# Optimization experiments

Hardware: AMD Instinct MI355X
Metric: run time of the kernel (lower is better)

Reference implementation:

```python
import jax, jax.numpy as jnp
import numpy as np

GW_EPS = 0.05
GW_SIGMA = 1.0
GW_OUTER_ITERS = 5
GW_SINK_ITERS = 20
N_HEADS = 8
EPS = 1e-8


def normalize_affinity(P):
    # symmetrize, scale to [0,1]
    P = 0.5 * (P + jnp.swapaxes(P, -1, -2))
    mx = jnp.max(P, axis=(-2, -1), keepdims=True)
    return P / jnp.maximum(mx, EPS)


def entropic_gw(C1, C2, a, b, eps, outer_iters, sink_iters):
    # C1: [B,H,S,S] node-space cost, C2: [B,H,K,K] slot-space cost
    # a: [B,H,S], b: [B,H,K] marginals. Square-loss entropic GW (Peyre et al.)
    T = a[..., :, None] * b[..., None, :]                      # [B,H,S,K]
    cC1 = jnp.einsum('bhij,bhj->bhi', C1 * C1, a)              # [B,H,S]
    cC2 = jnp.einsum('bhk,bhkl->bhl', b, C2 * C2)              # [B,H,K]
    const = cC1[..., :, None] + cC2[..., None, :]              # [B,H,S,K]
    tens = const
    for _ in range(outer_iters):
        tens = const - 2.0 * jnp.einsum('bhis,bhsk,bhlk->bhil', C1, T, C2)
        Kmat = jnp.exp(-tens / eps)
        u = jnp.ones_like(a)
        v = jnp.ones_like(b)
        def sink_step(carry, _):
            u, v = carry
            u = a / jnp.maximum(jnp.einsum('bhik,bhk->bhi', Kmat, v), 1e-30)
            v = b / jnp.maximum(jnp.einsum('bhik,bhi->bhk', Kmat, u), 1e-30)
            return (u, v), None
        (u, v), _ = jax.lax.scan(sink_step, (u, v), None, length=sink_iters)
        T = u[..., :, None] * Kmat * v[..., None, :]
    gw_val = jnp.sum(tens * T, axis=(-2, -1))                  # [B,H]
    return T, gw_val


def _forward(desc_embeddings, name_value_embeddings, shared_attn, prior_Q, DG, b, v_w, v_b):
    B, new_seq, D = name_value_embeddings.shape
    S = new_seq - 1
    H = N_HEADS
    hd = D // H

    # structural adjacency: CLS->Var on, Var->CLS off, Var-Var without self-loop
    var_adj = 1.0 - jnp.eye(S, dtype=name_value_embeddings.dtype)
    adj = jnp.zeros((new_seq, new_seq), dtype=name_value_embeddings.dtype)
    adj = adj.at[1:, 1:].set(var_adj)
    adj = adj.at[0, 1:].set(1.0)

    # Var-Var affinity from shared attention (detached in original)
    P_var = jax.lax.stop_gradient(shared_attn[:, :, 1:, 1:])   # [B,H,S,S]
    P_norm = normalize_affinity(P_var)
    DP = 1.0 - P_norm                                          # affinity -> distance

    deg_P = 0.5 * (P_norm.sum(-1) + P_norm.sum(-2))            # [B,H,S]
    a = deg_P / jnp.maximum(deg_P.sum(-1, keepdims=True), EPS)

    _, gw_val = entropic_gw(DP, DG, a, b, GW_EPS, GW_OUTER_ITERS, GW_SINK_ITERS)
    alpha = jnp.exp(-gw_val / GW_SIGMA)                        # [B,H] in (0,1]

    # sharpen prior Q by alpha (power sharpening + row renorm)
    Q_hat = jnp.power(jnp.maximum(prior_Q, EPS), 1.0 + alpha[..., None, None])
    Q_hat = Q_hat / jnp.maximum(Q_hat.sum(-1, keepdims=True), EPS)

    # embed Q_hat into CLS-augmented attention, mask, row-normalize
    slot = jnp.zeros((B, H, new_seq, new_seq), dtype=Q_hat.dtype)
    slot = slot.at[:, :, 1:, 1:].set(Q_hat)
    slot = slot.at[:, :, 0, 1:].set(1.0)
    slot = slot * adj[None, None]
    attn = slot / jnp.maximum(slot.sum(-1, keepdims=True), EPS)  # [B,H,S1,S1]

    v = name_value_embeddings @ v_w.T + v_b                    # [B,S1,D]
    v = v.reshape(B, new_seq, H, hd).transpose(0, 2, 1, 3)     # [B,H,S1,hd]
    context = jnp.einsum('bhij,bhjd->bhid', attn, v)
    basis_outputs = context.transpose(0, 2, 1, 3)              # [B,S1,H,hd]
    return basis_outputs, attn


def setup_inputs() -> dict:
    key = jax.random.key(0)
    ks = jax.random.split(key, 8)
    B, S1, D, H, K = 32, 385, 256, 8, 16
    S = S1 - 1
    desc = jax.random.normal(ks[0], (B, S, D), jnp.float32)
    nv = jax.random.normal(ks[1], (B, S1, D), jnp.float32)
    shared_attn = jax.nn.softmax(jax.random.normal(ks[2], (B, H, S1, S1), jnp.float32), axis=-1)
    prior_Q = jax.nn.softmax(jax.random.normal(ks[3], (B, H, S, S), jnp.float32), axis=-1)
    DG = jax.random.uniform(ks[4], (B, H, K, K), jnp.float32)
    DG = 0.5 * (DG + jnp.swapaxes(DG, -1, -2))
    b = jax.random.uniform(ks[5], (B, H, K), jnp.float32) + 0.1
    b = b / b.sum(-1, keepdims=True)
    v_w = jax.random.normal(ks[6], (D, D), jnp.float32) * (1.0 / np.sqrt(D))
    v_b = jnp.zeros((D,), jnp.float32)
    return {"desc_embeddings": desc, "name_value_embeddings": nv, "shared_attn": shared_attn,
            "prior_Q": prior_Q, "DG": DG, "b": b, "v_w": v_w, "v_b": v_b}


def reference(desc_embeddings, name_value_embeddings, shared_attn, prior_Q, DG, b, v_w, v_b):
    return _forward(desc_embeddings, name_value_embeddings, shared_attn, prior_Q, DG, b, v_w, v_b)
```

## Files before the change

kernel.cpp:

```cpp
#include <hip/hip_runtime.h>
#include <math.h>

constexpr int kS  = 384;
constexpr int kS1 = 385;
constexpr int kH  = 8;
constexpr int kB  = 32;
constexpr int kD  = 256;
constexpr float kEPS = 1e-8f;
constexpr float kNEG_INV_EPS_LOG2E = 28.853900817779268f;

__device__ __forceinline__ float waveReduceSum(float v) {
    #pragma unroll
    for (int m = 1; m < 64; m <<= 1) v += __shfl_xor(v, m);
    return v;
}
__device__ __forceinline__ float waveReduceMax(float v) {
    #pragma unroll
    for (int m = 1; m < 64; m <<= 1) v = fmaxf(v, __shfl_xor(v, m));
    return v;
}

__global__ __launch_bounds__(384) void k1_gw(
    const float* __restrict__ shared_attn,
    const float* __restrict__ DG,
    const float* __restrict__ bmarg,
    float* __restrict__ sym_ws,
    float* __restrict__ alpha_out)
{
    const int head = blockIdx.x;
    const int tid  = threadIdx.x;
    const int lane = tid & 63, wid = tid >> 6;

    __shared__ __align__(16) float uni[8320];
    __shared__ float Ks[kS * 17];
    __shared__ float ravu[kS];
    __shared__ float part[16 * 24];
    __shared__ float C2l[256];
    __shared__ float bl16[16], cb16[16], cC216[16], vls[16];
    __shared__ float wred[6];

    float* tA = uni;
    float* tB = uni + 4160;
    float* Ms = uni;

    const float* P = shared_attn + (size_t)head * (kS1 * kS1);
    float* SYM = sym_ws + (size_t)head * (kS1 * kS1);

    ravu[tid] = 0.f;
    if (tid < 256) C2l[tid] = DG[head * 256 + tid];
    if (tid >= 256 && tid < 272) bl16[tid - 256] = bmarg[head * 16 + (tid - 256)];
    __syncthreads();

    float mymax = -1e30f;
    for (int ti = 0; ti < 6; ++ti)
    for (int tj = ti; tj < 6; ++tj) {
        for (int e = tid; e < 4096; e += 384) {
            int r = e >> 6, c = e & 63;
            tA[r * 65 + c] = P[(ti * 64 + r + 1) * kS1 + (tj * 64 + c + 1)];
            tB[r * 65 + c] = P[(tj * 64 + r + 1) * kS1 + (ti * 64 + c + 1)];
        }
        __syncthreads();
        for (int e = tid; e < 4096; e += 384) {
            int r = e >> 6, c = e & 63;
            float v = 0.5f * (tA[r * 65 + c] + tB[c * 65 + r]);
            tA[r * 65 + c] = v;
            mymax = fmaxf(mymax, v);
        }
        __syncthreads();
        for (int e = tid; e < 4096; e += 384) {
            int r = e >> 6, c = e & 63;
            SYM[(ti * 64 + r) * kS + tj * 64 + c] = tA[r * 65 + c];
        }
        if (ti != tj) {
            for (int e = tid; e < 4096; e += 384) {
                int r = e >> 6, c = e & 63;
                SYM[(tj * 64 + r) * kS + ti * 64 + c] = tA[c * 65 + r];
            }
        }
        if (tid < 64) {
            int r = tid; float s = 0.f;
            #pragma unroll 8
            for (int c = 0; c < 64; ++c) s += tA[r * 65 + c];
            ravu[ti * 64 + r] += s;
        } else if (tid < 128 && ti != tj) {
            int c = tid - 64; float s = 0.f;
            #pragma unroll 8
            for (int r = 0; r < 64; ++r) s += tA[r * 65 + c];
            ravu[tj * 64 + c] += s;
        }
        __syncthreads();
    }

    float wm = waveReduceMax(mymax);
    if (lane == 0) wred[wid] = wm;
    __syncthreads();
    const float mx = fmaxf(fmaxf(fmaxf(wred[0], wred[1]), fmaxf(wred[2], wred[3])),
                           fmaxf(wred[4], wred[5]));
    float tloc = ravu[tid];
    float tw = waveReduceSum(tloc);
    __syncthreads();
    if (lane == 0) wred[wid] = tw;
    __syncthreads();
    const float total = wred[0] + wred[1] + wred[2] + wred[3] + wred[4] + wred[5];

    const float den_mx = fmaxf(mx, kEPS);
    const float inv_mx = 1.0f / den_mx;
    const float Sdeg   = total * inv_mx;
    const float den_a  = fmaxf(Sdeg, kEPS);
    const float a_reg  = (tloc * inv_mx) / den_a;
    __syncthreads();
    ravu[tid] = a_reg;

    if (tid < 16) {
        float cb = 0.f, cc2 = 0.f;
        #pragma unroll
        for (int k = 0; k < 16; ++k) {
            cb += bl16[k] * C2l[tid * 16 + k];
            float c2 = C2l[k * 16 + tid];
            cc2 = fmaf(bl16[k] * c2, c2, cc2);
        }
        cb16[tid] = cb; cC216[tid] = cc2;
    }
    __syncthreads();

    float t1 = 0.f, t2 = 0.f;
    {
        const float* symcol = SYM + tid;
        #pragma unroll 4
        for (int s = 0; s < kS; ++s) {
            float sym = symcol[s * kS];
            float dp  = fmaf(-inv_mx, sym, 1.0f);
            float as  = ravu[s];
            t1 = fmaf(dp, as, t1);
            t2 = fmaf(dp * dp, as, t2);
        }
    }
    const float cc1 = t2;
    #pragma unroll
    for (int l = 0; l < 16; ++l) {
        float tens = cc1 + cC216[l] - 2.0f * cb16[l] * t1;
        Ks[tid * 17 + l] = exp2f(tens * (-kNEG_INV_EPS_LOG2E));
    }

    float vreg[16];
    float u_i = 0.f;

    auto sinkhorn = [&]() {
        #pragma unroll
        for (int l = 0; l < 16; ++l) vreg[l] = 1.0f;
        for (int it = 0; it < 20; ++it) {
            float su = 0.f;
            #pragma unroll
            for (int l = 0; l < 16; ++l) su = fmaf(Ks[tid * 17 + l], vreg[l], su);
            u_i = a_reg / fmaxf(su, 1e-30f);
            ravu[tid] = u_i;
            __syncthreads();
            {
                int l = tid & 15, g = tid >> 4;
                float sv = 0.f;
                #pragma unroll
                for (int j = 0; j < 16; ++j)
                    sv = fmaf(Ks[(g * 16 + j) * 17 + l], ravu[g * 16 + j], sv);
                part[l * 24 + g] = sv;
            }
            __syncthreads();
            if (tid < 16) {
                float dn = 0.f;
                #pragma unroll
                for (int g = 0; g < 24; ++g) dn += part[tid * 24 + g];
                vls[tid] = bl16[tid] / fmaxf(dn, 1e-30f);
            }
            __syncthreads();
            #pragma unroll
            for (int l = 0; l < 16; ++l) vreg[l] = vls[l];
        }
    };

    __syncthreads();
    sinkhorn();

    float tens16[16];
    #pragma unroll
    for (int l = 0; l < 16; ++l) tens16[l] = 0.f;

    for (int outer = 1; outer < 5; ++outer) {
        {
            float wk[16];
            #pragma unroll
            for (int k = 0; k < 16; ++k) wk[k] = Ks[tid * 17 + k] * vreg[k];
            float m[16];
            #pragma unroll
            for (int l = 0; l < 16; ++l) {
                float acc = 0.f;
                #pragma unroll
                for (int k = 0; k < 16; ++k) acc = fmaf(wk[k], C2l[l * 16 + k], acc);
                m[l] = acc * u_i;
            }
            float4* Ms4 = (float4*)Ms;
            Ms4[tid * 4 + 0] = make_float4(m[0],  m[1],  m[2],  m[3]);
            Ms4[tid * 4 + 1] = make_float4(m[4],  m[5],  m[6],  m[7]);
            Ms4[tid * 4 + 2] = make_float4(m[8],  m[9],  m[10], m[11]);
            Ms4[tid * 4 + 3] = make_float4(m[12], m[13], m[14], m[15]);
        }
        __syncthreads();
        float rd[16];
        #pragma unroll
        for (int l = 0; l < 16; ++l) rd[l] = 0.f;
        {
            const float* symcol = SYM + tid;
            const float4* Ms4 = (const float4*)Ms;
            #pragma unroll 2
            for (int s = 0; s < kS; ++s) {
                float sym = symcol[s * kS];
                float dp  = fmaf(-inv_mx, sym, 1.0f);
                float4 m0 = Ms4[s * 4 + 0];
                float4 m1 = Ms4[s * 4 + 1];
                float4 m2 = Ms4[s * 4 + 2];
                float4 m3 = Ms4[s * 4 + 3];
                rd[0]  = fmaf(dp, m0.x, rd[0]);  rd[1]  = fmaf(dp, m0.y, rd[1]);
                rd[2]  = fmaf(dp, m0.z, rd[2]);  rd[3]  = fmaf(dp, m0.w, rd[3]);
                rd[4]  = fmaf(dp, m1.x, rd[4]);  rd[5]  = fmaf(dp, m1.y, rd[5]);
                rd[6]  = fmaf(dp, m1.z, rd[6]);  rd[7]  = fmaf(dp, m1.w, rd[7]);
                rd[8]  = fmaf(dp, m2.x, rd[8]);  rd[9]  = fmaf(dp, m2.y, rd[9]);
                rd[10] = fmaf(dp, m2.z, rd[10]); rd[11] = fmaf(dp, m2.w, rd[11]);
                rd[12] = fmaf(dp, m3.x, rd[12]); rd[13] = fmaf(dp, m3.y, rd[13]);
                rd[14] = fmaf(dp, m3.z, rd[14]); rd[15] = fmaf(dp, m3.w, rd[15]);
            }
        }
        #pragma unroll
        for (int l = 0; l < 16; ++l) {
            float tens = cc1 + cC216[l] - 2.0f * rd[l];
            if (outer == 4) tens16[l] = tens;
            Ks[tid * 17 + l] = exp2f(tens * (-kNEG_INV_EPS_LOG2E));
        }
        __syncthreads();
        sinkhorn();
    }

    float g = 0.f;
    #pragma unroll
    for (int l = 0; l < 16; ++l)
        g = fmaf(tens16[l] * Ks[tid * 17 + l], vreg[l], g);
    g *= u_i;
    float gww = waveReduceSum(g);
    __syncthreads();
    if (lane == 0) wred[wid] = gww;
    __syncthreads();
    if (tid == 0) {
        float gw = wred[0] + wred[1] + wred[2] + wred[3] + wred[4] + wred[5];
        alpha_out[head] = expf(-gw);
    }
}

__global__ __launch_bounds__(256) void k2_attn(
    const float* __restrict__ priorQ,
    const float* __restrict__ alpha_in,
    float* __restrict__ attn_out)
{
    const int tid  = threadIdx.x;
    const int lane = tid & 63, wid = tid >> 6;
    const int head = blockIdx.x / 97;
    const int i    = (blockIdx.x % 97) * 4 + wid;
    if (i >= kS1) return;
    float* row = attn_out + (size_t)head * (kS1 * kS1) + (size_t)i * kS1;
    if (i == 0) {
        const float val = 1.0f / 384.0f;
        for (int j = lane; j < kS1; j += 64) row[j] = (j == 0) ? 0.f : val;
        return;
    }
    const float e = 1.0f + alpha_in[head];
    const float* q = priorQ + (size_t)head * (kS * kS) + (size_t)(i - 1) * kS;
    float p[6];
    float loc = 0.f, locd = 0.f;
    #pragma unroll
    for (int k = 0; k < 6; ++k) {
        int j = lane + k * 64;
        float qv = fmaxf(q[j], kEPS);
        float pv = exp2f(e * log2f(qv));
        p[k] = pv;
        loc += pv;
        if (j == i - 1) locd = pv;
    }
    float sum = loc, pd = locd;
    #pragma unroll
    for (int m = 1; m < 64; m <<= 1) { sum += __shfl_xor(sum, m); pd += __shfl_xor(pd, m); }
    const float qsum  = fmaxf(sum, kEPS);
    const float srow  = (sum - pd) / qsum;
    const float scale = 1.0f / (qsum * fmaxf(srow, kEPS));
    if (lane == 0) row[0] = 0.f;
    #pragma unroll
    for (int k = 0; k < 6; ++k) {
        int j = lane + k * 64;
        row[1 + j] = (j == i - 1) ? 0.f : p[k] * scale;
    }
}

__global__ __launch_bounds__(256) void k3_vproj(
    const float* __restrict__ nv,
    const float* __restrict__ vw,
    const float* __restrict__ vb,
    float* __restrict__ vfull)
{
    __shared__ float At[64][17];
    __shared__ float Bt[256][17];
    const int tid = threadIdx.x;
    const int r0  = blockIdx.x * 64;
    const int tx  = tid & 31;
    const int ty  = tid >> 5;
    const int M   = kB * kS1;
    float acc[8][8];
    #pragma unroll
    for (int ri = 0; ri < 8; ++ri)
        #pragma unroll
        for (int ci = 0; ci < 8; ++ci) acc[ri][ci] = 0.f;

    for (int k0 = 0; k0 < 256; k0 += 16) {
        __syncthreads();
        for (int e = tid; e < 1024; e += 256) {
            int r = e >> 4, kk = e & 15;
            int rowi = r0 + r;
            At[r][kk] = (rowi < M) ? nv[rowi * 256 + k0 + kk] : 0.f;
        }
        for (int e = tid; e < 4096; e += 256) {
            int c = e >> 4, kk = e & 15;
            Bt[c][kk] = vw[c * 256 + k0 + kk];
        }
        __syncthreads();
        #pragma unroll
        for (int kk = 0; kk < 16; ++kk) {
            float av[8], bv[8];
            #pragma unroll
            for (int ri = 0; ri < 8; ++ri) av[ri] = At[ty * 8 + ri][kk];
            #pragma unroll
            for (int ci = 0; ci < 8; ++ci) bv[ci] = Bt[tx + 32 * ci][kk];
            #pragma unroll
            for (int ri = 0; ri < 8; ++ri)
                #pragma unroll
                for (int ci = 0; ci < 8; ++ci)
                    acc[ri][ci] = fmaf(av[ri], bv[ci], acc[ri][ci]);
        }
    }
    for (int ri = 0; ri < 8; ++ri) {
        int rowi = r0 + ty * 8 + ri;
        if (rowi < M) {
            #pragma unroll
            for (int ci = 0; ci < 8; ++ci) {
                int c = tx + 32 * ci;
                vfull[rowi * 256 + c] = acc[ri][ci] + vb[c];
            }
        }
    }
}

__global__ __launch_bounds__(256) void k4_ctx(
    const float* __restrict__ attn,
    const float* __restrict__ vfull,
    float* __restrict__ basis)
{
    __shared__ __align__(16) float at[8 * 32 * 28];
    __shared__ float vt[24 * 256];
    const int tid = threadIdx.x;
    const int bb  = blockIdx.y;
    const int i0  = blockIdx.x * 32;
    const int h   = tid >> 5;
    float acc[32];
    #pragma unroll
    for (int i = 0; i < 32; ++i) acc[i] = 0.f;
    const float* attnB = attn + (size_t)bb * kH * kS1 * kS1;
    const float* vB    = vfull + (size_t)bb * kS1 * 256;

    for (int j0 = 0; j0 < kS1; j0 += 24) {
        __syncthreads();
        for (int e = tid; e < 6144; e += 256) {
            int jj = e % 24, ii = (e / 24) & 31, hh = e / (24 * 32);
            int gi = i0 + ii, gj = j0 + jj;
            float v = (gi < kS1 && gj < kS1)
                      ? attnB[(size_t)hh * kS1 * kS1 + (size_t)gi * kS1 + gj] : 0.f;
            at[(hh * 32 + ii) * 28 + jj] = v;
        }
        for (int e = tid; e < 6144; e += 256) {
            int c = e & 255, jr = e >> 8;
            int gj = j0 + jr;
            vt[jr * 256 + c] = (gj < kS1) ? vB[gj * 256 + c] : 0.f;
        }
        __syncthreads();
        #pragma unroll
        for (int j4 = 0; j4 < 6; ++j4) {
            float v0 = vt[(j4 * 4 + 0) * 256 + tid];
            float v1 = vt[(j4 * 4 + 1) * 256 + tid];
            float v2 = vt[(j4 * 4 + 2) * 256 + tid];
            float v3 = vt[(j4 * 4 + 3) * 256 + tid];
            #pragma unroll
            for (int i = 0; i < 32; ++i) {
                float4 av = *(const float4*)&at[(h * 32 + i) * 28 + j4 * 4];
                acc[i] = fmaf(av.x, v0, fmaf(av.y, v1, fmaf(av.z, v2, fmaf(av.w, v3, acc[i]))));
            }
        }
    }
    for (int i = 0; i < 32; ++i) {
        int gi = i0 + i;
        if (gi < kS1) basis[((size_t)bb * kS1 + gi) * 256 + tid] = acc[i];
    }
}

extern "C" void kernel_launch(void* const* d_in, const int* in_sizes, int n_in,
                              void* d_out, int out_size, void* d_ws, size_t ws_size,
                              hipStream_t stream) {
    (void)in_sizes; (void)n_in; (void)out_size; (void)ws_size;
    const float* nv    = (const float*)d_in[1];
    const float* sattn = (const float*)d_in[2];
    const float* pq    = (const float*)d_in[3];
    const float* dg    = (const float*)d_in[4];
    const float* bm    = (const float*)d_in[5];
    const float* vw    = (const float*)d_in[6];
    const float* vb    = (const float*)d_in[7];

    float* out   = (float*)d_out;
    float* basis = out;
    float* attn  = out + (size_t)kB * kS1 * kD;
    float* alpha = (float*)d_ws;
    float* vfull = (float*)((char*)d_ws + 4096);

    k1_gw<<<256, 384, 0, stream>>>(sattn, dg, bm, attn, alpha);
    k2_attn<<<256 * 97, 256, 0, stream>>>(pq, alpha, attn);
    k3_vproj<<<193, 256, 0, stream>>>(nv, vw, vb, vfull);
    k4_ctx<<<dim3(13, 32), 256, 0, stream>>>(attn, vfull, basis);
}
```

Measured before the change: 1.336 ms.

## Split per-head GW solver into multi-block kernels and retile context matmul

The monolithic per-head GW kernel becomes several launches. Symmetrization runs over 21 tile pairs per head, with the max and row sums combined through atomics. The SYM-column reductions (t1/t2, and rd for each outer iteration) are split over 4 blocks per head with atomic accumulation, and a small per-head solve kernel runs Sinkhorn between them. The initial t1/cc1 are rewritten algebraically from raw sums of SYM and SYM². k4_ctx is also retiled per head with 4x4 register blocking. This spreads the memory-bound SYM streaming over far more blocks than 256, at the cost of more launches, memsets, atomics, and scratch stored in the output buffer before it is overwritten.

```diff
diff --git a/kernel.cpp b/kernel.cpp
--- a/kernel.cpp
+++ b/kernel.cpp
@@ -20,97 +20,137 @@
     return v;
 }
 
-__global__ __launch_bounds__(384) void k1_gw(
-    const float* __restrict__ shared_attn,
-    const float* __restrict__ DG,
-    const float* __restrict__ bmarg,
-    float* __restrict__ sym_ws,
-    float* __restrict__ alpha_out)
+__global__ __launch_bounds__(256) void kA_sym(
+    const float* __restrict__ P_, float* __restrict__ sym,
+    float* __restrict__ r_ws, unsigned int* __restrict__ mxbits)
+{
+    const int head = blockIdx.y;
+    int p = blockIdx.x, ti = 0;
+    while (p >= 6 - ti) { p -= 6 - ti; ++ti; }
+    const int tj = ti + p;
+    const int tid = threadIdx.x;
+    __shared__ float Bt[64 * 65];
+    __shared__ float St[64 * 65];
+    const float* P = P_ + (size_t)head * (kS1 * kS1);
+    float* SYM = sym + (size_t)head * (kS1 * kS1);
+
+    #pragma unroll
+    for (int e = tid; e < 4096; e += 256) {
+        int rr = e >> 6, cc = e & 63;
+        Bt[rr * 65 + cc] = P[(size_t)(tj * 64 + rr + 1) * kS1 + ti * 64 + cc + 1];
+    }
+    __syncthreads();
+    float mymax = 0.f;
+    #pragma unroll
+    for (int e = tid; e < 4096; e += 256) {
+        int rr = e >> 6, cc = e & 63;
+        float s = 0.5f * (P[(size_t)(ti * 64 + rr + 1) * kS1 + tj * 64 + cc + 1] + Bt[cc * 65 + rr]);
+        St[rr * 65 + cc] = s;
+        mymax = fmaxf(mymax, s);
+        SYM[(size_t)(ti * 64 + rr) * kS + tj * 64 + cc] = s;
+    }
+    __syncthreads();
+    if (ti != tj) {
+        #pragma unroll
+        for (int e = tid; e < 4096; e += 256) {
+            int rr = e >> 6, cc = e & 63;
+            SYM[(size_t)(tj * 64 + rr) * kS + ti * 64 + cc] = St[cc * 65 + rr];
+        }
+    }
+    float wm = waveReduceMax(mymax);
+    if ((tid & 63) == 0) atomicMax(mxbits + head, __float_as_uint(wm));
+    if (tid < 64) {
+        float s = 0.f;
+        #pragma unroll 8
+        for (int c = 0; c < 64; ++c) s += St[tid * 65 + c];
+        atomicAdd(r_ws + head * kS + ti * 64 + tid, s);
+    } else if (tid < 128 && ti != tj) {
+        int c = tid - 64; float s = 0.f;
+        #pragma unroll 8
+        for (int rr2 = 0; rr2 < 64; ++rr2) s += St[rr2 * 65 + c];
+        atomicAdd(r_ws + head * kS + tj * 64 + c, s);
+    }
+}
+
+__global__ __launch_bounds__(384) void kB_t(
+    const float* __restrict__ sym, const float* __restrict__ r_ws,
+    float* __restrict__ s1acc, float* __restrict__ s2acc)
+{
+    const int head = blockIdx.y;
+    const int s0 = blockIdx.x * 96;
+    const int tid = threadIdx.x;
+    __shared__ float rs[96];
+    if (tid < 96) rs[tid] = r_ws[head * kS + s0 + tid];
+    __syncthreads();
+    const float* SYM = sym + (size_t)head * (kS1 * kS1) + (size_t)s0 * kS + tid;
+    float s1 = 0.f, s2 = 0.f;
+    #pragma unroll 4
+    for (int k = 0; k < 96; ++k) {
+        float sy = SYM[(size_t)k * kS];
+        float rv = rs[k];
+        s1 = fmaf(sy, rv, s1);
+        s2 = fmaf(sy * sy, rv, s2);
+    }
+    atomicAdd(s1acc + head * kS + tid, s1);
+    atomicAdd(s2acc + head * kS + tid, s2);
+}
+
+__global__ __launch_bounds__(384) void kD_stream(
+    const float* __restrict__ sym, const float* __restrict__ Ms,
+    const unsigned int* __restrict__ mxbits, float* __restrict__ rd_acc)
+{
+    const int head = blockIdx.y;
+    const int s0 = blockIdx.x * 96;
+    const int tid = threadIdx.x;
+    __shared__ __align__(16) float MsS[96 * 16];
+    ((float4*)MsS)[tid] = ((const float4*)(Ms + (size_t)head * 6144 + s0 * 16))[tid];
+    __syncthreads();
+    const float inv_mx = 1.0f / fmaxf(__uint_as_float(mxbits[head]), kEPS);
+    const float* SYM = sym + (size_t)head * (kS1 * kS1) + (size_t)s0 * kS + tid;
+    float rd[16];
+    #pragma unroll
+    for (int l = 0; l < 16; ++l) rd[l] = 0.f;
+    const float4* Ms4 = (const float4*)MsS;
+    #pragma unroll 2
+    for (int k = 0; k < 96; ++k) {
+        float dp = fmaf(-inv_mx, SYM[(size_t)k * kS], 1.0f);
+        float4 m0 = Ms4[k * 4 + 0];
+        float4 m1 = Ms4[k * 4 + 1];
+        float4 m2 = Ms4[k * 4 + 2];
+        float4 m3 = Ms4[k * 4 + 3];
+        rd[0]  = fmaf(dp, m0.x, rd[0]);  rd[1]  = fmaf(dp, m0.y, rd[1]);
+        rd[2]  = fmaf(dp, m0.z, rd[2]);  rd[3]  = fmaf(dp, m0.w, rd[3]);
+        rd[4]  = fmaf(dp, m1.x, rd[4]);  rd[5]  = fmaf(dp, m1.y, rd[5]);
+        rd[6]  = fmaf(dp, m1.z, rd[6]);  rd[7]  = fmaf(dp, m1.w, rd[7]);
+        rd[8]  = fmaf(dp, m2.x, rd[8]);  rd[9]  = fmaf(dp, m2.y, rd[9]);
+        rd[10] = fmaf(dp, m2.z, rd[10]); rd[11] = fmaf(dp, m2.w, rd[11]);
+        rd[12] = fmaf(dp, m3.x, rd[12]); rd[13] = fmaf(dp, m3.y, rd[13]);
+        rd[14] = fmaf(dp, m3.z, rd[14]); rd[15] = fmaf(dp, m3.w, rd[15]);
+    }
+    float* dst = rd_acc + (size_t)head * 6144 + tid * 16;
+    #pragma unroll
+    for (int l = 0; l < 16; ++l) atomicAdd(dst + l, rd[l]);
+}
+
+__global__ __launch_bounds__(384) void kSolve(
+    const float* __restrict__ DG, const float* __restrict__ bmarg,
+    float* __restrict__ a_ws, const unsigned int* __restrict__ mxbits,
+    float* __restrict__ cc1_ws, const float* __restrict__ s2acc,
+    float* __restrict__ rd_acc, float* __restrict__ Ms,
+    float* __restrict__ alpha_out, int mode)
 {
     const int head = blockIdx.x;
     const int tid  = threadIdx.x;
     const int lane = tid & 63, wid = tid >> 6;
-
-    __shared__ __align__(16) float uni[8320];
     __shared__ float Ks[kS * 17];
     __shared__ float ravu[kS];
     __shared__ float part[16 * 24];
     __shared__ float C2l[256];
-    __shared__ float bl16[16], cb16[16], cC216[16], vls[16];
-    __shared__ float wred[6];
-
-    float* tA = uni;
-    float* tB = uni + 4160;
-    float* Ms = uni;
-
-    const float* P = shared_attn + (size_t)head * (kS1 * kS1);
-    float* SYM = sym_ws + (size_t)head * (kS1 * kS1);
-
-    ravu[tid] = 0.f;
+    __shared__ float bl16[16], cb16[16], cC216[16], vls[16], wred[6];
+
     if (tid < 256) C2l[tid] = DG[head * 256 + tid];
     if (tid >= 256 && tid < 272) bl16[tid - 256] = bmarg[head * 16 + (tid - 256)];
     __syncthreads();
-
-    float mymax = -1e30f;
-    for (int ti = 0; ti < 6; ++ti)
-    for (int tj = ti; tj < 6; ++tj) {
-        for (int e = tid; e < 4096; e += 384) {
-            int r = e >> 6, c = e & 63;
-            tA[r * 65 + c] = P[(ti * 64 + r + 1) * kS1 + (tj * 64 + c + 1)];
-            tB[r * 65 + c] = P[(tj * 64 + r + 1) * kS1 + (ti * 64 + c + 1)];
-        }
-        __syncthreads();
-        for (int e = tid; e < 4096; e += 384) {
-            int r = e >> 6, c = e & 63;
-            float v = 0.5f * (tA[r * 65 + c] + tB[c * 65 + r]);
-            tA[r * 65 + c] = v;
-            mymax = fmaxf(mymax, v);
-        }
-        __syncthreads();
-        for (int e = tid; e < 4096; e += 384) {
-            int r = e >> 6, c = e & 63;
-            SYM[(ti * 64 + r) * kS + tj * 64 + c] = tA[r * 65 + c];
-        }
-        if (ti != tj) {
-            for (int e = tid; e < 4096; e += 384) {
-                int r = e >> 6, c = e & 63;
-                SYM[(tj * 64 + r) * kS + ti * 64 + c] = tA[c * 65 + r];
-            }
-        }
-        if (tid < 64) {
-            int r = tid; float s = 0.f;
-            #pragma unroll 8
-            for (int c = 0; c < 64; ++c) s += tA[r * 65 + c];
-            ravu[ti * 64 + r] += s;
-        } else if (tid < 128 && ti != tj) {
-            int c = tid - 64; float s = 0.f;
-            #pragma unroll 8
-            for (int r = 0; r < 64; ++r) s += tA[r * 65 + c];
-            ravu[tj * 64 + c] += s;
-        }
-        __syncthreads();
-    }
-
-    float wm = waveReduceMax(mymax);
-    if (lane == 0) wred[wid] = wm;
-    __syncthreads();
-    const float mx = fmaxf(fmaxf(fmaxf(wred[0], wred[1]), fmaxf(wred[2], wred[3])),
-                           fmaxf(wred[4], wred[5]));
-    float tloc = ravu[tid];
-    float tw = waveReduceSum(tloc);
-    __syncthreads();
-    if (lane == 0) wred[wid] = tw;
-    __syncthreads();
-    const float total = wred[0] + wred[1] + wred[2] + wred[3] + wred[4] + wred[5];
-
-    const float den_mx = fmaxf(mx, kEPS);
-    const float inv_mx = 1.0f / den_mx;
-    const float Sdeg   = total * inv_mx;
-    const float den_a  = fmaxf(Sdeg, kEPS);
-    const float a_reg  = (tloc * inv_mx) / den_a;
-    __syncthreads();
-    ravu[tid] = a_reg;
-
     if (tid < 16) {
         float cb = 0.f, cc2 = 0.f;
         #pragma unroll
@@ -121,134 +161,113 @@
         }
         cb16[tid] = cb; cC216[tid] = cc2;
     }
-    __syncthreads();
-
-    float t1 = 0.f, t2 = 0.f;
-    {
-        const float* symcol = SYM + tid;
-        #pragma unroll 4
-        for (int s = 0; s < kS; ++s) {
-            float sym = symcol[s * kS];
-            float dp  = fmaf(-inv_mx, sym, 1.0f);
-            float as  = ravu[s];
-            t1 = fmaf(dp, as, t1);
-            t2 = fmaf(dp * dp, as, t2);
-        }
-    }
-    const float cc1 = t2;
-    #pragma unroll
-    for (int l = 0; l < 16; ++l) {
-        float tens = cc1 + cC216[l] - 2.0f * cb16[l] * t1;
-        Ks[tid * 17 + l] = exp2f(tens * (-kNEG_INV_EPS_LOG2E));
-    }
+
+    float a_i, cc1, u_i = 0.f;
+    float tens16[16];
+
+    if (mode == 0) {
+        float r_i = a_ws[head * kS + tid];
+        float tw = waveReduceSum(r_i);
+        if (lane == 0) wred[wid] = tw;
+        __syncthreads();
+        const float total = wred[0] + wred[1] + wred[2] + wred[3] + wred[4] + wred[5];
+        const float inv_mx = 1.0f / fmaxf(__uint_as_float(mxbits[head]), kEPS);
+        const float den_a = fmaxf(total * inv_mx, kEPS);
+        a_i = (r_i * inv_mx) / den_a;
+        a_ws[head * kS + tid] = a_i;
+        const float S1 = cc1_ws[head * kS + tid];
+        const float S2 = s2acc[head * kS + tid];
+        const float sc = inv_mx / den_a;
+        const float t1 = (total - inv_mx * S1) * sc;
+        cc1 = fmaf(inv_mx * inv_mx, S2, fmaf(-2.0f * inv_mx, S1, total)) * sc;
+        cc1_ws[head * kS + tid] = cc1;
+        #pragma unroll
+        for (int l = 0; l < 16; ++l)
+            tens16[l] = cc1 + cC216[l] - 2.0f * cb16[l] * t1;
+    } else {
+        a_i = a_ws[head * kS + tid];
+        cc1 = cc1_ws[head * kS + tid];
+        float4* rp = (float4*)(rd_acc + (size_t)head * 6144 + tid * 16);
+        float4 rd0 = rp[0], rd1 = rp[1], rd2 = rp[2], rd3 = rp[3];
+        if (mode == 1) {
+            float4 z = make_float4(0.f, 0.f, 0.f, 0.f);
+            rp[0] = z; rp[1] = z; rp[2] = z; rp[3] = z;
+        }
+        __syncthreads();
+        tens16[0]  = cc1 + cC216[0]  - 2.f * rd0.x; tens16[1]  = cc1 + cC216[1]  - 2.f * rd0.y;
+        tens16[2]  = cc1 + cC216[2]  - 2.f * rd0.z; tens16[3]  = cc1 + cC216[3]  - 2.f * rd0.w;
+        tens16[4]  = cc1 + cC216[4]  - 2.f * rd1.x; tens16[5]  = cc1 + cC216[5]  - 2.f * rd1.y;
+        tens16[6]  = cc1 + cC216[6]  - 2.f * rd1.z; tens16[7]  = cc1 + cC216[7]  - 2.f * rd1.w;
+        tens16[8]  = cc1 + cC216[8]  - 2.f * rd2.x; tens16[9]  = cc1 + cC216[9]  - 2.f * rd2.y;
+        tens16[10] = cc1 + cC216[10] - 2.f * rd2.z; tens16[11] = cc1 + cC216[11] - 2.f * rd2.w;
+        tens16[12] = cc1 + cC216[12] - 2.f * rd3.x; tens16[13] = cc1 + cC216[13] - 2.f * rd3.y;
+        tens16[14] = cc1 + cC216[14] - 2.f * rd3.z; tens16[15] = cc1 + cC216[15] - 2.f * rd3.w;
+    }
+
+    #pragma unroll
+    for (int l = 0; l < 16; ++l)
+        Ks[tid * 17 + l] = exp2f(tens16[l] * (-kNEG_INV_EPS_LOG2E));
+    __syncthreads();
 
     float vreg[16];
-    float u_i = 0.f;
-
-    auto sinkhorn = [&]() {
-        #pragma unroll
-        for (int l = 0; l < 16; ++l) vreg[l] = 1.0f;
-        for (int it = 0; it < 20; ++it) {
-            float su = 0.f;
-            #pragma unroll
-            for (int l = 0; l < 16; ++l) su = fmaf(Ks[tid * 17 + l], vreg[l], su);
-            u_i = a_reg / fmaxf(su, 1e-30f);
-            ravu[tid] = u_i;
-            __syncthreads();
-            {
-                int l = tid & 15, g = tid >> 4;
-                float sv = 0.f;
-                #pragma unroll
-                for (int j = 0; j < 16; ++j)
-                    sv = fmaf(Ks[(g * 16 + j) * 17 + l], ravu[g * 16 + j], sv);
-                part[l * 24 + g] = sv;
-            }
-            __syncthreads();
-            if (tid < 16) {
-                float dn = 0.f;
-                #pragma unroll
-                for (int g = 0; g < 24; ++g) dn += part[tid * 24 + g];
-                vls[tid] = bl16[tid] / fmaxf(dn, 1e-30f);
-            }
-            __syncthreads();
-            #pragma unroll
-            for (int l = 0; l < 16; ++l) vreg[l] = vls[l];
-        }
-    };
-
-    __syncthreads();
-    sinkhorn();
-
-    float tens16[16];
-    #pragma unroll
-    for (int l = 0; l < 16; ++l) tens16[l] = 0.f;
-
-    for (int outer = 1; outer < 5; ++outer) {
+    #pragma unroll
+    for (int l = 0; l < 16; ++l) vreg[l] = 1.0f;
+    for (int it = 0; it < 20; ++it) {
+        float su = 0.f;
+        #pragma unroll
+        for (int l = 0; l < 16; ++l) su = fmaf(Ks[tid * 17 + l], vreg[l], su);
+        u_i = a_i / fmaxf(su, 1e-30f);
+        ravu[tid] = u_i;
+        __syncthreads();
         {
-            float wk[16];
-            #pragma unroll
-            for (int k = 0; k < 16; ++k) wk[k] = Ks[tid * 17 + k] * vreg[k];
-            float m[16];
-            #pragma unroll
-            for (int l = 0; l < 16; ++l) {
-                float acc = 0.f;
-                #pragma unroll
-                for (int k = 0; k < 16; ++k) acc = fmaf(wk[k], C2l[l * 16 + k], acc);
-                m[l] = acc * u_i;
-            }
-            float4* Ms4 = (float4*)Ms;
-            Ms4[tid * 4 + 0] = make_float4(m[0],  m[1],  m[2],  m[3]);
-            Ms4[tid * 4 + 1] = make_float4(m[4],  m[5],  m[6],  m[7]);
-            Ms4[tid * 4 + 2] = make_float4(m[8],  m[9],  m[10], m[11]);
-            Ms4[tid * 4 + 3] = make_float4(m[12], m[13], m[14], m[15]);
-        }
-        __syncthreads();
-        float rd[16];
-        #pragma unroll
-        for (int l = 0; l < 16; ++l) rd[l] = 0.f;
-        {
-            const float* symcol = SYM + tid;
-            const float4* Ms4 = (const float4*)Ms;
-            #pragma unroll 2
-            for (int s = 0; s < kS; ++s) {
-                float sym = symcol[s * kS];
-                float dp  = fmaf(-inv_mx, sym, 1.0f);
-                float4 m0 = Ms4[s * 4 + 0];
-                float4 m1 = Ms4[s * 4 + 1];
-                float4 m2 = Ms4[s * 4 + 2];
-                float4 m3 = Ms4[s * 4 + 3];
-                rd[0]  = fmaf(dp, m0.x, rd[0]);  rd[1]  = fmaf(dp, m0.y, rd[1]);
-                rd[2]  = fmaf(dp, m0.z, rd[2]);  rd[3]  = fmaf(dp, m0.w, rd[3]);
-                rd[4]  = fmaf(dp, m1.x, rd[4]);  rd[5]  = fmaf(dp, m1.y, rd[5]);
-                rd[6]  = fmaf(dp, m1.z, rd[6]);  rd[7]  = fmaf(dp, m1.w, rd[7]);
-                rd[8]  = fmaf(dp, m2.x, rd[8]);  rd[9]  = fmaf(dp, m2.y, rd[9]);
-                rd[10] = fmaf(dp, m2.z, rd[10]); rd[11] = fmaf(dp, m2.w, rd[11]);
-                rd[12] = fmaf(dp, m3.x, rd[12]); rd[13] = fmaf(dp, m3.y, rd[13]);
-                rd[14] = fmaf(dp, m3.z, rd[14]); rd[15] = fmaf(dp, m3.w, rd[15]);
-            }
-        }
+            int l = tid & 15, g = tid >> 4;
+            float sv = 0.f;
+            #pragma unroll
+            for (int j = 0; j < 16; ++j)
+                sv = fmaf(Ks[(g * 16 + j) * 17 + l], ravu[g * 16 + j], sv);
+            part[l * 24 + g] = sv;
+        }
+        __syncthreads();
+        if (tid < 16) {
+            float dn = 0.f;
+            #pragma unroll
+            for (int g = 0; g < 24; ++g) dn += part[tid * 24 + g];
+            vls[tid] = bl16[tid] / fmaxf(dn, 1e-30f);
+        }
+        __syncthreads();
+        #pragma unroll
+        for (int l = 0; l < 16; ++l) vreg[l] = vls[l];
+    }
+
+    if (mode <= 1) {
+        float wk[16];
+        #pragma unroll
+        for (int k = 0; k < 16; ++k) wk[k] = Ks[tid * 17 + k] * vreg[k];
+        float m[16];
         #pragma unroll
         for (int l = 0; l < 16; ++l) {
-            float tens = cc1 + cC216[l] - 2.0f * rd[l];
-            if (outer == 4) tens16[l] = tens;
-            Ks[tid * 17 + l] = exp2f(tens * (-kNEG_INV_EPS_LOG2E));
-        }
-        __syncthreads();
-        sinkhorn();
-    }
-
-    float g = 0.f;
-    #pragma unroll
-    for (int l = 0; l < 16; ++l)
-        g = fmaf(tens16[l] * Ks[tid * 17 + l], vreg[l], g);
-    g *= u_i;
-    float gww = waveReduceSum(g);
-    __syncthreads();
-    if (lane == 0) wred[wid] = gww;
-    __syncthreads();
-    if (tid == 0) {
-        float gw = wred[0] + wred[1] + wred[2] + wred[3] + wred[4] + wred[5];
-        alpha_out[head] = expf(-gw);
+            float acc = 0.f;
+            #pragma unroll
+            for (int k = 0; k < 16; ++k) acc = fmaf(wk[k], C2l[l * 16 + k], acc);
+            m[l] = acc * u_i;
+        }
+        float4* Ms4 = (float4*)(Ms + (size_t)head * 6144 + tid * 16);
+        Ms4[0] = make_float4(m[0],  m[1],  m[2],  m[3]);
+        Ms4[1] = make_float4(m[4],  m[5],  m[6],  m[7]);
+        Ms4[2] = make_float4(m[8],  m[9],  m[10], m[11]);
+        Ms4[3] = make_float4(m[12], m[13], m[14], m[15]);
+    } else {
+        float g = 0.f;
+        #pragma unroll
+        for (int l = 0; l < 16; ++l)
+            g = fmaf(tens16[l] * Ks[tid * 17 + l], vreg[l], g);
+        g *= u_i;
+        float gww = waveReduceSum(g);
+        __syncthreads();
+        if (lane == 0) wred[wid] = gww;
+        __syncthreads();
+        if (tid == 0)
+            alpha_out[head] = expf(-(wred[0] + wred[1] + wred[2] + wred[3] + wred[4] + wred[5]));
     }
 }
 
@@ -296,10 +315,8 @@
 }
 
 __global__ __launch_bounds__(256) void k3_vproj(
-    const float* __restrict__ nv,
-    const float* __restrict__ vw,
-    const float* __restrict__ vb,
-    float* __restrict__ vfull)
+    const float* __restrict__ nv, const float* __restrict__ vw,
+    const float* __restrict__ vb, float* __restrict__ vfull)
 {
     __shared__ float At[64][17];
     __shared__ float Bt[256][17];
@@ -353,53 +370,56 @@
 }
 
 __global__ __launch_bounds__(256) void k4_ctx(
-    const float* __restrict__ attn,
-    const float* __restrict__ vfull,
+    const float* __restrict__ attn, const float* __restrict__ vfull,
     float* __restrict__ basis)
 {
-    __shared__ __align__(16) float at[8 * 32 * 28];
-    __shared__ float vt[24 * 256];
     const int tid = threadIdx.x;
-    const int bb  = blockIdx.y;
-    const int i0  = blockIdx.x * 32;
-    const int h   = tid >> 5;
-    float acc[32];
-    #pragma unroll
-    for (int i = 0; i < 32; ++i) acc[i] = 0.f;
-    const float* attnB = attn + (size_t)bb * kH * kS1 * kS1;
-    const float* vB    = vfull + (size_t)bb * kS1 * 256;
-
-    for (int j0 = 0; j0 < kS1; j0 += 24) {
-        __syncthreads();
-        for (int e = tid; e < 6144; e += 256) {
-            int jj = e % 24, ii = (e / 24) & 31, hh = e / (24 * 32);
-            int gi = i0 + ii, gj = j0 + jj;
-            float v = (gi < kS1 && gj < kS1)
-                      ? attnB[(size_t)hh * kS1 * kS1 + (size_t)gi * kS1 + gj] : 0.f;
-            at[(hh * 32 + ii) * 28 + jj] = v;
-        }
-        for (int e = tid; e < 6144; e += 256) {
-            int c = e & 255, jr = e >> 8;
-            int gj = j0 + jr;
-            vt[jr * 256 + c] = (gj < kS1) ? vB[gj * 256 + c] : 0.f;
-        }
-        __syncthreads();
-        #pragma unroll
-        for (int j4 = 0; j4 < 6; ++j4) {
-            float v0 = vt[(j4 * 4 + 0) * 256 + tid];
-            float v1 = vt[(j4 * 4 + 1) * 256 + tid];
-            float v2 = vt[(j4 * 4 + 2) * 256 + tid];
-            float v3 = vt[(j4 * 4 + 3) * 256 + tid];
-            #pragma unroll
-            for (int i = 0; i < 32; ++i) {
-                float4 av = *(const float4*)&at[(h * 32 + i) * 28 + j4 * 4];
-                acc[i] = fmaf(av.x, v0, fmaf(av.y, v1, fmaf(av.z, v2, fmaf(av.w, v3, acc[i]))));
-            }
-        }
-    }
-    for (int i = 0; i < 32; ++i) {
-        int gi = i0 + i;
-        if (gi < kS1) basis[((size_t)bb * kS1 + gi) * 256 + tid] = acc[i];
+    const int it0 = blockIdx.x * 128;
+    const int h   = blockIdx.y;
+    const int bb  = blockIdx.z;
+    __shared__ __align__(16) float at[16][132];
+    __shared__ __align__(16) float vs[16][36];
+    const float* A = attn + (size_t)(bb * kH + h) * (kS1 * kS1);
+    const float* V = vfull + (size_t)bb * kS1 * 256 + h * 32;
+    const int itr = tid >> 3;
+    const int ct  = tid & 7;
+    float4 acc0 = make_float4(0, 0, 0, 0), acc1 = acc0, acc2 = acc0, acc3 = acc0;
+
+    for (int j0 = 0; j0 < kS1; j0 += 16) {
+        __syncthreads();
+        #pragma unroll
+        for (int e = tid; e < 2048; e += 256) {
+            int jj = e & 15, ii = e >> 4;
+            int gi = it0 + ii, gj = j0 + jj;
+            at[jj][ii] = (gi < kS1 && gj < kS1) ? A[(size_t)gi * kS1 + gj] : 0.f;
+        }
+        #pragma unroll
+        for (int e = tid; e < 512; e += 256) {
+            int cc = e & 31, jj = e >> 5;
+            int gj = j0 + jj;
+            vs[jj][cc] = (gj < kS1) ? V[(size_t)gj * 256 + cc] : 0.f;
+        }
+        __syncthreads();
+        #pragma unroll
+        for (int jj = 0; jj < 16; ++jj) {
+            float4 vv = *(const float4*)&vs[jj][ct * 4];
+            float4 aa = *(const float4*)&at[jj][itr * 4];
+            acc0.x = fmaf(aa.x, vv.x, acc0.x); acc0.y = fmaf(aa.x, vv.y, acc0.y);
+            acc0.z = fmaf(aa.x, vv.z, acc0.z); acc0.w = fmaf(aa.x, vv.w, acc0.w);
+            acc1.x = fmaf(aa.y, vv.x, acc1.x); acc1.y = fmaf(aa.y, vv.y, acc1.y);
+            acc1.z = fmaf(aa.y, vv.z, acc1.z); acc1.w = fmaf(aa.y, vv.w, acc1.w);
+            acc2.x = fmaf(aa.z, vv.x, acc2.x); acc2.y = fmaf(aa.z, vv.y, acc2.y);
+            acc2.z = fmaf(aa.z, vv.z, acc2.z); acc2.w = fmaf(aa.z, vv.w, acc2.w);
+            acc3.x = fmaf(aa.w, vv.x, acc3.x); acc3.y = fmaf(aa.w, vv.y, acc3.y);
+            acc3.z = fmaf(aa.w, vv.z, acc3.z); acc3.w = fmaf(aa.w, vv.w, acc3.w);
+        }
+    }
+    float4 accs[4] = {acc0, acc1, acc2, acc3};
+    #pragma unroll
+    for (int r = 0; r < 4; ++r) {
+        int gi = it0 + itr * 4 + r;
+        if (gi < kS1)
+            *(float4*)&basis[((size_t)bb * kS1 + gi) * 256 + h * 32 + ct * 4] = accs[r];
     }
 }
 
@@ -417,12 +437,30 @@
 
     float* out   = (float*)d_out;
     float* basis = out;
-    float* attn  = out + (size_t)kB * kS1 * kD;
-    float* alpha = (float*)d_ws;
-    float* vfull = (float*)((char*)d_ws + 4096);
-
-    k1_gw<<<256, 384, 0, stream>>>(sattn, dg, bm, attn, alpha);
-    k2_attn<<<256 * 97, 256, 0, stream>>>(pq, alpha, attn);
+    float* attnO = out + (size_t)kB * kS1 * kD;
+
+    float*        r_ws   = basis;
+    unsigned int* mxbits = (unsigned int*)(basis + 98304);
+    float*        s1acc  = basis + 98560;
+    float*        s2acc  = basis + 196864;
+    float*        alpha  = basis + 295168;
+
+    float* rd_acc = (float*)d_ws;
+    float* Ms     = rd_acc + 1572864;
+    float* vfull  = (float*)d_ws;
+
+    hipMemsetAsync(basis, 0, 295424 * 4, stream);
+    hipMemsetAsync(rd_acc, 0, 6291456, stream);
+
+    kA_sym<<<dim3(21, 256), 256, 0, stream>>>(sattn, attnO, r_ws, mxbits);
+    kB_t<<<dim3(4, 256), 384, 0, stream>>>(attnO, r_ws, s1acc, s2acc);
+    kSolve<<<256, 384, 0, stream>>>(dg, bm, r_ws, mxbits, s1acc, s2acc, rd_acc, Ms, alpha, 0);
+    for (int it = 1; it <= 4; ++it) {
+        kD_stream<<<dim3(4, 256), 384, 0, stream>>>(attnO, Ms, mxbits, rd_acc);
+        kSolve<<<256, 384, 0, stream>>>(dg, bm, r_ws, mxbits, s1acc, s2acc, rd_acc, Ms, alpha,
+                                        it < 4 ? 1 : 2);
+    }
+    k2_attn<<<256 * 97, 256, 0, stream>>>(pq, alpha, attnO);
     k3_vproj<<<193, 256, 0, stream>>>(nv, vw, vb, vfull);
-    k4_ctx<<<dim3(13, 32), 256, 0, stream>>>(attn, vfull, basis);
-}
+    k4_ctx<<<dim3(4, 8, 32), 256, 0, stream>>>(attnO, vfull, basis);
+}
```

After: 2.185 ms. 63.6% more time.
